# Kernel tuning notes

Hardware: AMD Instinct MI355X
Metric: run time of the kernel (lower is better)

## Reference

```python
import jax, jax.numpy as jnp
import numpy as np

B, L, D_IN = 2048, 512, 32
PRED_LEN = 96
COND = 128      # cond_dim (z_dim)
XPROJ = 128     # x_proj_dim defaults to cond_dim
ODE_H = 128     # ode_hidden
TDIM = 128      # time_dim
HID = 256       # hidden of final MLP
N_STEPS = 32    # fixed-step RK4 steps over t in [0,1] (stands in for adaptive dopri5)
LN_EPS = 1e-5


def _linear(x, w, b):
    return x @ w.T + b


def _layernorm(x, g, b):
    mu = jnp.mean(x, axis=-1, keepdims=True)
    var = jnp.var(x, axis=-1, keepdims=True)
    return (x - mu) * jax.lax.rsqrt(var + LN_EPS) * g + b


def _interp(x_seq, t):
    # linear interp over sequence dim: x_seq (B,L,D), scalar t in [0,1] -> (B,D)
    Ls = x_seq.shape[1]
    pos = jnp.clip(t, 0.0, 1.0) * (Ls - 1)
    i0 = jnp.clip(jnp.floor(pos).astype(jnp.int32), 0, Ls - 1)
    i1 = jnp.clip(i0 + 1, 0, Ls - 1)
    w = (pos - i0.astype(pos.dtype))
    x0 = jax.lax.dynamic_index_in_dim(x_seq, i0, axis=1, keepdims=False)
    x1 = jax.lax.dynamic_index_in_dim(x_seq, i1, axis=1, keepdims=False)
    return (1.0 - w) * x0 + w * x1


def setup_inputs() -> dict:
    key = jax.random.key(0)
    ks = jax.random.split(key, 16)

    def kaiming(k, shape):
        return jax.random.normal(k, shape, jnp.float32) * np.float32(np.sqrt(2.0 / shape[-1]))

    IN_F = PRED_LEN * D_IN + COND + TDIM   # 3328
    OUT_F = PRED_LEN * D_IN                # 3072
    return {
        "x_t": jax.random.normal(ks[0], (B, PRED_LEN, D_IN), jnp.float32),
        "past": jax.random.normal(ks[1], (B, L, D_IN), jnp.float32),
        "t": jax.random.randint(ks[2], (B,), 0, 1000),
        "xproj_w": kaiming(ks[3], (XPROJ, D_IN)), "xproj_b": jnp.zeros((XPROJ,), jnp.float32),
        "z0_w": kaiming(ks[4], (COND, XPROJ)), "z0_b": jnp.zeros((COND,), jnp.float32),
        "ln_g": jnp.ones((COND,), jnp.float32), "ln_b": jnp.zeros((COND,), jnp.float32),
        "w1": kaiming(ks[5], (ODE_H, COND + XPROJ)), "b1": jnp.zeros((ODE_H,), jnp.float32),
        "w2": kaiming(ks[6], (ODE_H, ODE_H)), "b2": jnp.zeros((ODE_H,), jnp.float32),
        "w3": kaiming(ks[7], (COND, ODE_H)), "b3": jnp.zeros((COND,), jnp.float32),
        "fw1": kaiming(ks[8], (HID, IN_F)), "fb1": jnp.zeros((HID,), jnp.float32),
        "fw2": kaiming(ks[9], (HID, HID)), "fb2": jnp.zeros((HID,), jnp.float32),
        "fw3": kaiming(ks[10], (OUT_F, HID)), "fb3": jnp.zeros((OUT_F,), jnp.float32),
    }


def _time_emb(t):
    half = TDIM // 2
    freqs = jnp.exp(-np.float32(np.log(10000.0)) * jnp.arange(half, dtype=jnp.float32) / (half - 1))
    args = t.astype(jnp.float32)[:, None] * freqs[None, :]
    return jnp.concatenate([jnp.sin(args), jnp.cos(args)], axis=1)  # (B, TDIM)


def _forward(x_t, past, t, xproj_w, xproj_b, z0_w, z0_b, ln_g, ln_b,
             w1, b1, w2, b2, w3, b3, fw1, fb1, fw2, fb2, fw3, fb3):
    Bn = x_t.shape[0]
    x_seq = _linear(past, xproj_w, xproj_b)           # (B,L,XPROJ)
    z0 = _linear(x_seq[:, 0, :], z0_w, z0_b)          # (B,COND)

    def odef(tt, z):
        xt = _interp(x_seq, tt)                       # (B,XPROJ)
        zn = _layernorm(z, ln_g, ln_b)
        h = jnp.concatenate([zn, xt], axis=-1)
        h = jax.nn.silu(_linear(h, w1, b1))
        h = jax.nn.silu(_linear(h, w2, b2))
        return _linear(h, w3, b3)                     # (B,COND)

    dt = jnp.float32(1.0 / N_STEPS)

    def step(z, tt):
        k1 = odef(tt, z)
        k2 = odef(tt + dt * 0.5, z + dt * 0.5 * k1)
        k3 = odef(tt + dt * 0.5, z + dt * 0.5 * k2)
        k4 = odef(tt + dt, z + dt * k3)
        return z + (dt / 6.0) * (k1 + 2.0 * k2 + 2.0 * k3 + k4), None

    ts = jnp.arange(N_STEPS, dtype=jnp.float32) * dt
    cond, _ = jax.lax.scan(step, z0, ts)              # zT (B,COND)

    temb = _time_emb(t)                               # (B,TDIM)
    x_flat = x_t.reshape(Bn, -1)                      # (B,PRED_LEN*D_IN)
    h = jnp.concatenate([x_flat, cond, temb], axis=1)
    h = jax.nn.silu(_linear(h, fw1, fb1))
    h = jax.nn.silu(_linear(h, fw2, fb2))
    eps = _linear(h, fw3, fb3)
    return eps.reshape(Bn, PRED_LEN, D_IN)


def reference(x_t, past, t, xproj_w, xproj_b, z0_w, z0_b, ln_g, ln_b,
              w1, b1, w2, b2, w3, b3, fw1, fb1, fw2, fb2, fw3, fb3):
    return _forward(x_t, past, t, xproj_w, xproj_b, z0_w, z0_b, ln_g, ln_b,
                    w1, b1, w2, b2, w3, b3, fw1, fb1, fw2, fb2, fw3, fb3)
```

## Files before the change

### kernel.cpp

```cpp
#include <hip/hip_runtime.h>
#include <math.h>

typedef _Float16 h8f16 __attribute__((ext_vector_type(8)));
typedef _Float16 h4f16 __attribute__((ext_vector_type(4)));
typedef _Float16 h2f16 __attribute__((ext_vector_type(2)));
typedef float f32x4 __attribute__((ext_vector_type(4)));

#define MFMA16(a, b, c) __builtin_amdgcn_mfma_f32_16x16x32_f16((a), (b), (c), 0, 0, 0)

__device__ __forceinline__ float silu_f(float v) {
    return v * __builtin_amdgcn_rcpf(1.0f + __expf(-v));
}

__device__ __forceinline__ void bar_lds() {
    asm volatile("s_waitcnt lgkmcnt(0)" ::: "memory");
    __builtin_amdgcn_s_barrier();
    __builtin_amdgcn_sched_barrier(0);
}

__global__ __launch_bounds__(512, 1) void fat_kernel(
    const float* __restrict__ past,
    const float* __restrict__ xproj_w, const float* __restrict__ xproj_b,
    const float* __restrict__ z0_w, const float* __restrict__ z0_b,
    const float* __restrict__ ln_g, const float* __restrict__ ln_b,
    const float* __restrict__ w1, const float* __restrict__ b1,
    const float* __restrict__ w2, const float* __restrict__ b2,
    const float* __restrict__ w3, const float* __restrict__ b3,
    const float* __restrict__ x_t, const float* __restrict__ fw1,
    const int* __restrict__ tvals,
    float* __restrict__ zbuf, float* __restrict__ h1pre,
    _Float16* __restrict__ tbuf)
{
    __shared__ union {
        struct {
            _Float16 hbuf[16][136];
            _Float16 h1S[16][136];
            _Float16 h2S[16][136];
            float    pS[16][33];
            float    x0S[16][128];
            float    zS0[16][129];
        } ode;
        struct {
            _Float16 aS[128][40];
            _Float16 wS[64][40];
        } gx;
    } sm;

    const int tid = threadIdx.x;

    if (blockIdx.x >= 192) {
        const int t = blockIdx.x - 192;
        for (int c = 0; c < 8; ++c) {
            const int chunk = t * 512 + tid + c * 4096;
            const int b  = chunk >> 4;
            const int j0 = (chunk & 15) * 8;
            const float tv = (float)tvals[b];
            h8f16 v;
#pragma unroll
            for (int j = 0; j < 8; ++j) {
                const int jj  = j0 + j;
                const int idx = (jj < 64) ? jj : jj - 64;
                const float fr = expf(-9.210340371976184f * (float)idx * (1.0f / 63.0f));
                const float a  = tv * fr;
                v[j] = (_Float16)((jj < 64) ? sinf(a) : cosf(a));
            }
            *(h8f16*)&tbuf[(long)b * 128 + j0] = v;
        }
        return;
    }

    if (blockIdx.x >= 128) {
        const int g  = blockIdx.x - 128;
        const int mb = (g >> 2) * 128;
        const int nb = (g & 3) * 64;
        const int lane = tid & 63, wid = tid >> 6;
        const int lrow = lane & 15, lhi = lane >> 4;
        f32x4 acc[4];
#pragma unroll
        for (int nt = 0; nt < 4; ++nt) acc[nt] = (f32x4){0, 0, 0, 0};

        const int sra = tid >> 2, ska = (tid & 3) * 8;
        const int srw = tid >> 3, skw = (tid & 7) * 4;

        for (int k0 = 0; k0 < 3072; k0 += 32) {
            {
                const float* s = x_t + (long)(mb + sra) * 3072 + k0 + ska;
                const f32x4 u0 = *(const f32x4*)s;
                const f32x4 u1 = *(const f32x4*)(s + 4);
                h8f16 v;
#pragma unroll
                for (int j = 0; j < 4; ++j) { v[j] = (_Float16)u0[j]; v[4 + j] = (_Float16)u1[j]; }
                *(h8f16*)&sm.gx.aS[sra][ska] = v;
            }
            {
                const float* s = fw1 + (long)(nb + srw) * 3328 + k0 + skw;
                const f32x4 u = *(const f32x4*)s;
                h4f16 v;
#pragma unroll
                for (int j = 0; j < 4; ++j) v[j] = (_Float16)u[j];
                *(h4f16*)&sm.gx.wS[srw][skw] = v;
            }
            __syncthreads();
            const h8f16 a = *(const h8f16*)&sm.gx.aS[wid * 16 + lrow][lhi * 8];
#pragma unroll
            for (int nt = 0; nt < 4; ++nt) {
                const h8f16 bfr = *(const h8f16*)&sm.gx.wS[nt * 16 + lrow][lhi * 8];
                acc[nt] = MFMA16(a, bfr, acc[nt]);
            }
            __syncthreads();
        }
#pragma unroll
        for (int nt = 0; nt < 4; ++nt) {
            const int cc = nb + nt * 16 + lrow;
#pragma unroll
            for (int j = 0; j < 4; ++j) {
                const int rr = mb + wid * 16 + lhi * 4 + j;
                h1pre[(long)rr * 256 + cc] = acc[nt][j];
            }
        }
        return;
    }

    _Float16 (&hbuf)[16][136] = sm.ode.hbuf;
    _Float16 (&h1S)[16][136]  = sm.ode.h1S;
    _Float16 (&h2S)[16][136]  = sm.ode.h2S;
    float    (&pS)[16][33]    = sm.ode.pS;
    float    (&x0S)[16][128]  = sm.ode.x0S;
    float    (&zS0)[16][129]  = sm.ode.zS0;

    const int wid  = tid >> 6;
    const int lane = tid & 63;
    const int lrow = lane & 15;
    const int lhi  = lane >> 4;
    const int b0   = blockIdx.x * 16;
    const int nc   = wid * 16 + lrow;
    const int koff = lhi * 8;

    h8f16 w1f[4], wcf, w2f[4], w3f[4];
    float b1t, b2r, b3r;
    {
#pragma unroll
        for (int ks = 0; ks < 4; ++ks) {
            h8f16 v1, v2, v3;
#pragma unroll
            for (int j = 0; j < 8; ++j) {
                const int k = ks * 32 + koff + j;
                v1[j] = (_Float16)(w1[nc * 256 + k] * ln_g[k]);
                v2[j] = (_Float16)w2[nc * 128 + k];
                v3[j] = (_Float16)w3[nc * 128 + k];
            }
            w1f[ks] = v1; w2f[ks] = v2; w3f[ks] = v3;
        }
        float wc[8] = {0, 0, 0, 0, 0, 0, 0, 0};
        float bc = 0.0f, bb = 0.0f;
        const float* w1a = w1 + nc * 256;
        const float* w1b = w1a + 128;
#pragma unroll 4
        for (int k = 0; k < 128; ++k) {
            const float a = w1b[k];
            bc += a * xproj_b[k];
            bb += w1a[k] * ln_b[k];
            const float* xr = xproj_w + k * 32 + koff;
#pragma unroll
            for (int j = 0; j < 8; ++j) wc[j] += a * xr[j];
        }
        h8f16 v;
#pragma unroll
        for (int j = 0; j < 8; ++j) v[j] = (_Float16)wc[j];
        wcf = v;
        b1t = b1[nc] + bc + bb;
        b2r = b2[nc]; b3r = b3[nc];
    }

    if (tid < 512) {
        pS[tid >> 5][tid & 31] = past[(long)(b0 + (tid >> 5)) * 16384 + (tid & 31)];
    }
    __syncthreads();
    {
        const int r  = tid >> 5;
        const int c0 = (tid & 31) * 4;
#pragma unroll
        for (int cc = 0; cc < 4; ++cc) {
            const int kc = c0 + cc;
            float s = xproj_b[kc];
            const float* xr = xproj_w + kc * 32;
#pragma unroll
            for (int c = 0; c < 32; ++c) s += pS[r][c] * xr[c];
            x0S[r][kc] = s;
        }
    }
    __syncthreads();
    {
        const int nn = tid & 127;
        const int r0 = (tid >> 7) * 4;
        for (int p = 0; p < 4; ++p) {
            const int r = r0 + p;
            float s = z0_b[nn];
            const float* zr = z0_w + nn * 128;
            for (int k = 0; k < 128; ++k) s += x0S[r][k] * zr[k];
            zS0[r][nn] = s;
        }
    }
    __syncthreads();

    float zc[4], krk[4];
#pragma unroll
    for (int j = 0; j < 4; ++j) {
        zc[j] = zS0[4 * lhi + j][nc];
        hbuf[4 * lhi + j][nc] = (_Float16)zc[j];
    }

    const float DT = 1.0f / 32.0f;

    f32x4 s0a, s0b, s1a, s1b;
    auto stage = [&](int e) {
        const float pos = (float)e * 7.984375f;
        const int i0 = (int)pos;
        const int i1 = (i0 < 511) ? i0 + 1 : 511;
        const float* base = past + (long)(b0 + lrow) * 16384;
        const float* p0 = base + i0 * 32 + koff;
        const float* p1 = base + i1 * 32 + koff;
        s0a = *(const f32x4*)p0; s0b = *(const f32x4*)(p0 + 4);
        s1a = *(const f32x4*)p1; s1b = *(const f32x4*)(p1 + 4);
    };
    auto blend = [&](int e) -> h8f16 {
        const float pos = (float)e * 7.984375f;
        const float w = pos - floorf(pos);
        h8f16 r;
#pragma unroll
        for (int j = 0; j < 4; ++j) {
            r[j]     = (_Float16)(s0a[j] + w * (s1a[j] - s0a[j]));
            r[4 + j] = (_Float16)(s0b[j] + w * (s1b[j] - s0b[j]));
        }
        return r;
    };

    const h2f16 one2 = {(_Float16)1.0f, (_Float16)1.0f};

    auto phaseA = [&](h8f16 bxc) {
        h8f16 xf[4];
#pragma unroll
        for (int ks = 0; ks < 4; ++ks)
            xf[ks] = *(const h8f16*)&hbuf[lrow][ks * 32 + koff];
        float s0 = 0.f, s1 = 0.f, q0 = 0.f, q1 = 0.f;
#pragma unroll
        for (int ks = 0; ks < 4; ++ks) {
#pragma unroll
            for (int p = 0; p < 4; ++p) {
                const h2f16 x2 = {xf[ks][2 * p], xf[ks][2 * p + 1]};
                if (p & 1) {
                    s1 = __builtin_amdgcn_fdot2(x2, one2, s1, false);
                    q1 = __builtin_amdgcn_fdot2(x2, x2, q1, false);
                } else {
                    s0 = __builtin_amdgcn_fdot2(x2, one2, s0, false);
                    q0 = __builtin_amdgcn_fdot2(x2, x2, q0, false);
                }
            }
        }
        float s = s0 + s1, q = q0 + q1;
        s += __shfl_xor(s, 16); q += __shfl_xor(q, 16);
        s += __shfl_xor(s, 32); q += __shfl_xor(q, 32);
        const float mu  = s * (1.0f / 128.0f);
        const float var = q * (1.0f / 128.0f) - mu * mu;
        const float inv = 1.0f / sqrtf(var + 1e-5f);
        const _Float16 ih = (_Float16)inv;
        const _Float16 mh = (_Float16)(-mu * inv);
        h8f16 ip, mp;
#pragma unroll
        for (int j = 0; j < 8; ++j) { ip[j] = ih; mp[j] = mh; }
        f32x4 acc = {0, 0, 0, 0};
#pragma unroll
        for (int ks = 0; ks < 4; ++ks) {
            const h8f16 az = xf[ks] * ip + mp;
            acc = MFMA16(az, w1f[ks], acc);
        }
        acc = MFMA16(bxc, wcf, acc);
#pragma unroll
        for (int j = 0; j < 4; ++j)
            h1S[4 * lhi + j][nc] = (_Float16)silu_f(acc[j] + b1t);
    };
    auto phaseB = [&]() {
        f32x4 acc = {0, 0, 0, 0};
#pragma unroll
        for (int ks = 0; ks < 4; ++ks) {
            const h8f16 a = *(const h8f16*)&h1S[lrow][ks * 32 + koff];
            acc = MFMA16(a, w2f[ks], acc);
        }
#pragma unroll
        for (int j = 0; j < 4; ++j)
            h2S[4 * lhi + j][nc] = (_Float16)silu_f(acc[j] + b2r);
    };
    auto phaseC = [&]() -> f32x4 {
        f32x4 acc = {0, 0, 0, 0};
#pragma unroll
        for (int ks = 0; ks < 4; ++ks) {
            const h8f16 a = *(const h8f16*)&h2S[lrow][ks * 32 + koff];
            acc = MFMA16(a, w3f[ks], acc);
        }
#pragma unroll
        for (int j = 0; j < 4; ++j) acc[j] += b3r;
        return acc;
    };

    stage(0);
    h8f16 bxc = blend(0);
    __syncthreads();

#pragma unroll 1
    for (int st = 0; st < 32; ++st) {
        const int e1 = 2 * st + 1, e2 = 2 * st + 2;
        phaseA(bxc);
        stage(e1);
        bar_lds();
        phaseB(); bar_lds();
        {
            const f32x4 k = phaseC();
#pragma unroll
            for (int j = 0; j < 4; ++j) {
                krk[j] = k[j];
                hbuf[4 * lhi + j][nc] = (_Float16)(zc[j] + 0.5f * DT * k[j]);
            }
        }
        bar_lds();
        bxc = blend(e1);
        phaseA(bxc); bar_lds();
        phaseB(); bar_lds();
        {
            const f32x4 k = phaseC();
#pragma unroll
            for (int j = 0; j < 4; ++j) {
                krk[j] += 2.0f * k[j];
                hbuf[4 * lhi + j][nc] = (_Float16)(zc[j] + 0.5f * DT * k[j]);
            }
        }
        bar_lds();
        phaseA(bxc);
        stage(e2);
        bar_lds();
        phaseB(); bar_lds();
        {
            const f32x4 k = phaseC();
#pragma unroll
            for (int j = 0; j < 4; ++j) {
                krk[j] += 2.0f * k[j];
                hbuf[4 * lhi + j][nc] = (_Float16)(zc[j] + DT * k[j]);
            }
        }
        bar_lds();
        bxc = blend(e2);
        phaseA(bxc); bar_lds();
        phaseB(); bar_lds();
        {
            const f32x4 k = phaseC();
#pragma unroll
            for (int j = 0; j < 4; ++j) {
                zc[j] += (DT / 6.0f) * (krk[j] + k[j]);
                hbuf[4 * lhi + j][nc] = (_Float16)zc[j];
            }
        }
        bar_lds();
    }

#pragma unroll
    for (int j = 0; j < 4; ++j)
        zbuf[(long)(b0 + 4 * lhi + j) * 128 + nc] = zc[j];
}

__global__ __launch_bounds__(256) void gemm1c_kernel(
    const float* __restrict__ cond, const _Float16* __restrict__ tbuf,
    const float* __restrict__ fw1, const float* __restrict__ fb1,
    const float* __restrict__ h1pre, _Float16* __restrict__ h1)
{
    __shared__ _Float16 aS[64][40];
    __shared__ _Float16 wS[64][40];
    const int mb = blockIdx.x * 64, nb = blockIdx.y * 64;
    const int tid = threadIdx.x, lane = tid & 63, wq = tid >> 6;
    const int lrow = lane & 15, lhi = lane >> 4;
    f32x4 acc[4];
#pragma unroll
    for (int nt = 0; nt < 4; ++nt) acc[nt] = (f32x4){0, 0, 0, 0};

    const int sr = tid >> 2;
    const int sk = (tid & 3) * 8;

    for (int k0 = 0; k0 < 256; k0 += 32) {
        if (k0 < 128) {
            const float* s = cond + (long)(mb + sr) * 128 + k0 + sk;
            const f32x4 u0 = *(const f32x4*)s;
            const f32x4 u1 = *(const f32x4*)(s + 4);
            h8f16 v;
#pragma unroll
            for (int j = 0; j < 4; ++j) { v[j] = (_Float16)u0[j]; v[4 + j] = (_Float16)u1[j]; }
            *(h8f16*)&aS[sr][sk] = v;
        } else {
            *(h8f16*)&aS[sr][sk] =
                *(const h8f16*)&tbuf[(long)(mb + sr) * 128 + (k0 - 128) + sk];
        }
        {
            const float* s = fw1 + (long)(nb + sr) * 3328 + 3072 + k0 + sk;
            h8f16 v;
#pragma unroll
            for (int j = 0; j < 8; ++j) v[j] = (_Float16)s[j];
            *(h8f16*)&wS[sr][sk] = v;
        }
        __syncthreads();
        const h8f16 a = *(const h8f16*)&aS[wq * 16 + lrow][lhi * 8];
#pragma unroll
        for (int nt = 0; nt < 4; ++nt) {
            const h8f16 bfr = *(const h8f16*)&wS[nt * 16 + lrow][lhi * 8];
            acc[nt] = MFMA16(a, bfr, acc[nt]);
        }
        __syncthreads();
    }

#pragma unroll
    for (int nt = 0; nt < 4; ++nt) {
        const int cc = nb + nt * 16 + lrow;
        const float bv = fb1[cc];
#pragma unroll
        for (int j = 0; j < 4; ++j) {
            const int rr = mb + wq * 16 + lhi * 4 + j;
            const float v = acc[nt][j] + h1pre[(long)rr * 256 + cc] + bv;
            h1[(long)rr * 256 + cc] = (_Float16)silu_f(v);
        }
    }
}

template <bool SILU, bool OUT_F16>
__global__ __launch_bounds__(256) void gemm_f16(
    const _Float16* __restrict__ A, const float* __restrict__ W,
    const float* __restrict__ bias, void* __restrict__ out,
    int M, int N, int K)
{
    __shared__ _Float16 aS[64][40];
    __shared__ _Float16 wS[64][40];
    const int mb = blockIdx.x * 64, nb = blockIdx.y * 64;
    const int tid = threadIdx.x, lane = tid & 63, wq = tid >> 6;
    const int lrow = lane & 15, lhi = lane >> 4;
    f32x4 acc[4];
#pragma unroll
    for (int nt = 0; nt < 4; ++nt) acc[nt] = (f32x4){0, 0, 0, 0};

    const int sr = tid >> 2;
    const int sk = (tid & 3) * 8;

    for (int k0 = 0; k0 < K; k0 += 32) {
        {
            h8f16 v = *(const h8f16*)&A[(long)(mb + sr) * K + k0 + sk];
            *(h8f16*)&aS[sr][sk] = v;
        }
        {
            const float* s = &W[(long)(nb + sr) * K + k0 + sk];
            h8f16 v;
#pragma unroll
            for (int j = 0; j < 8; ++j) v[j] = (_Float16)s[j];
            *(h8f16*)&wS[sr][sk] = v;
        }
        __syncthreads();
        h8f16 a = *(const h8f16*)&aS[wq * 16 + lrow][lhi * 8];
#pragma unroll
        for (int nt = 0; nt < 4; ++nt) {
            h8f16 bfr = *(const h8f16*)&wS[nt * 16 + lrow][lhi * 8];
            acc[nt] = MFMA16(a, bfr, acc[nt]);
        }
        __syncthreads();
    }

#pragma unroll
    for (int nt = 0; nt < 4; ++nt) {
        const int cc = nb + nt * 16 + lrow;
        const float bv = bias[cc];
#pragma unroll
        for (int j = 0; j < 4; ++j) {
            const int rr = mb + wq * 16 + lhi * 4 + j;
            float v = acc[nt][j] + bv;
            if (SILU) v = silu_f(v);
            if (OUT_F16) ((_Float16*)out)[(long)rr * N + cc] = (_Float16)v;
            else         ((float*)out)[(long)rr * N + cc] = v;
        }
    }
}

extern "C" void kernel_launch(void* const* d_in, const int* in_sizes, int n_in,
                              void* d_out, int out_size, void* d_ws, size_t ws_size,
                              hipStream_t stream)
{
    const float* x_t     = (const float*)d_in[0];
    const float* past    = (const float*)d_in[1];
    const int*   tvals   = (const int*)d_in[2];
    const float* xproj_w = (const float*)d_in[3];
    const float* xproj_b = (const float*)d_in[4];
    const float* z0_w    = (const float*)d_in[5];
    const float* z0_b    = (const float*)d_in[6];
    const float* ln_g    = (const float*)d_in[7];
    const float* ln_b    = (const float*)d_in[8];
    const float* w1      = (const float*)d_in[9];
    const float* b1      = (const float*)d_in[10];
    const float* w2      = (const float*)d_in[11];
    const float* b2      = (const float*)d_in[12];
    const float* w3      = (const float*)d_in[13];
    const float* b3      = (const float*)d_in[14];
    const float* fw1     = (const float*)d_in[15];
    const float* fb1     = (const float*)d_in[16];
    const float* fw2     = (const float*)d_in[17];
    const float* fb2     = (const float*)d_in[18];
    const float* fw3     = (const float*)d_in[19];
    const float* fb3     = (const float*)d_in[20];

    char* ws = (char*)d_ws;
    float*     zbuf  = (float*)ws;
    _Float16*  tbuf  = (_Float16*)(ws + (1 << 20));
    float*     h1pre = (float*)(ws + 2 * (1 << 20));
    _Float16*  h1    = (_Float16*)(ws + 4 * (1 << 20));
    _Float16*  h2    = (_Float16*)(ws + 5 * (1 << 20));

    fat_kernel<<<200, 512, 0, stream>>>(past, xproj_w, xproj_b, z0_w, z0_b,
                                        ln_g, ln_b, w1, b1, w2, b2, w3, b3,
                                        x_t, fw1, tvals, zbuf, h1pre, tbuf);

    gemm1c_kernel<<<dim3(32, 4), 256, 0, stream>>>(zbuf, tbuf, fw1, fb1, h1pre, h1);

    gemm_f16<true,  true ><<<dim3(32, 4),  256, 0, stream>>>(h1, fw2, fb2, h2, 2048, 256, 256);
    gemm_f16<false, false><<<dim3(32, 48), 256, 0, stream>>>(h2, fw3, fb3, d_out, 2048, 3072, 256);
}
```

Measured before the change: 368.6 us.

## Split fat kernel; run ODE with one wave per tile without barriers

```diff
diff --git a/kernel.cpp b/kernel.cpp
--- a/kernel.cpp
+++ b/kernel.cpp
@@ -2,7 +2,6 @@
 #include <math.h>
 
 typedef _Float16 h8f16 __attribute__((ext_vector_type(8)));
-typedef _Float16 h4f16 __attribute__((ext_vector_type(4)));
 typedef _Float16 h2f16 __attribute__((ext_vector_type(2)));
 typedef float f32x4 __attribute__((ext_vector_type(4)));
 
@@ -12,205 +11,115 @@
     return v * __builtin_amdgcn_rcpf(1.0f + __expf(-v));
 }
 
-__device__ __forceinline__ void bar_lds() {
-    asm volatile("s_waitcnt lgkmcnt(0)" ::: "memory");
-    __builtin_amdgcn_s_barrier();
-    __builtin_amdgcn_sched_barrier(0);
-}
-
-__global__ __launch_bounds__(512, 1) void fat_kernel(
+__global__ __launch_bounds__(128) void z0wc_kernel(
     const float* __restrict__ past,
-    const float* __restrict__ xproj_w, const float* __restrict__ xproj_b,
-    const float* __restrict__ z0_w, const float* __restrict__ z0_b,
-    const float* __restrict__ ln_g, const float* __restrict__ ln_b,
-    const float* __restrict__ w1, const float* __restrict__ b1,
+    const float* __restrict__ xw, const float* __restrict__ xb,
+    const float* __restrict__ zw, const float* __restrict__ zb,
+    const float* __restrict__ w1, const float* __restrict__ lnb,
+    const float* __restrict__ b1,
+    float* __restrict__ zbuf, float* __restrict__ wcb, float* __restrict__ b1tb)
+{
+    const int tid = threadIdx.x;
+    if (blockIdx.x == 2048) {
+        const int n = tid;
+        float wc[32];
+#pragma unroll
+        for (int c = 0; c < 32; ++c) wc[c] = 0.0f;
+        float bc = 0.0f, bb = 0.0f;
+        const float* w1a = w1 + n * 256;
+        const float* w1b = w1a + 128;
+        for (int k = 0; k < 128; ++k) {
+            const float a = w1b[k];
+            bc += a * xb[k];
+            bb += w1a[k] * lnb[k];
+            const float* xr = xw + k * 32;
+#pragma unroll
+            for (int c = 0; c < 32; ++c) wc[c] = fmaf(a, xr[c], wc[c]);
+        }
+#pragma unroll
+        for (int c = 0; c < 32; ++c) wcb[n * 32 + c] = wc[c];
+        b1tb[n] = b1[n] + bc + bb;
+        return;
+    }
+    __shared__ float p[32];
+    __shared__ float x0[128];
+    const int b = blockIdx.x;
+    if (tid < 32) p[tid] = past[(long)b * 16384 + tid];
+    __syncthreads();
+    float s = xb[tid];
+#pragma unroll
+    for (int c = 0; c < 32; ++c) s += p[c] * xw[tid * 32 + c];
+    x0[tid] = s;
+    __syncthreads();
+    float z = zb[tid];
+    for (int k = 0; k < 128; ++k) z += x0[k] * zw[tid * 128 + k];
+    zbuf[(long)b * 128 + tid] = z;
+}
+
+__global__ __launch_bounds__(64, 1) void ode_kernel(
+    const float* __restrict__ past,
+    const float* __restrict__ ln_g,
+    const float* __restrict__ w1,
+    const float* __restrict__ wcb, const float* __restrict__ b1tb,
     const float* __restrict__ w2, const float* __restrict__ b2,
     const float* __restrict__ w3, const float* __restrict__ b3,
-    const float* __restrict__ x_t, const float* __restrict__ fw1,
-    const int* __restrict__ tvals,
-    float* __restrict__ zbuf, float* __restrict__ h1pre,
-    _Float16* __restrict__ tbuf)
-{
-    __shared__ union {
-        struct {
-            _Float16 hbuf[16][136];
-            _Float16 h1S[16][136];
-            _Float16 h2S[16][136];
-            float    pS[16][33];
-            float    x0S[16][128];
-            float    zS0[16][129];
-        } ode;
-        struct {
-            _Float16 aS[128][40];
-            _Float16 wS[64][40];
-        } gx;
-    } sm;
-
-    const int tid = threadIdx.x;
-
-    if (blockIdx.x >= 192) {
-        const int t = blockIdx.x - 192;
-        for (int c = 0; c < 8; ++c) {
-            const int chunk = t * 512 + tid + c * 4096;
-            const int b  = chunk >> 4;
-            const int j0 = (chunk & 15) * 8;
-            const float tv = (float)tvals[b];
-            h8f16 v;
-#pragma unroll
-            for (int j = 0; j < 8; ++j) {
-                const int jj  = j0 + j;
-                const int idx = (jj < 64) ? jj : jj - 64;
-                const float fr = expf(-9.210340371976184f * (float)idx * (1.0f / 63.0f));
-                const float a  = tv * fr;
-                v[j] = (_Float16)((jj < 64) ? sinf(a) : cosf(a));
-            }
-            *(h8f16*)&tbuf[(long)b * 128 + j0] = v;
-        }
-        return;
-    }
-
-    if (blockIdx.x >= 128) {
-        const int g  = blockIdx.x - 128;
-        const int mb = (g >> 2) * 128;
-        const int nb = (g & 3) * 64;
-        const int lane = tid & 63, wid = tid >> 6;
-        const int lrow = lane & 15, lhi = lane >> 4;
-        f32x4 acc[4];
-#pragma unroll
-        for (int nt = 0; nt < 4; ++nt) acc[nt] = (f32x4){0, 0, 0, 0};
-
-        const int sra = tid >> 2, ska = (tid & 3) * 8;
-        const int srw = tid >> 3, skw = (tid & 7) * 4;
-
-        for (int k0 = 0; k0 < 3072; k0 += 32) {
-            {
-                const float* s = x_t + (long)(mb + sra) * 3072 + k0 + ska;
-                const f32x4 u0 = *(const f32x4*)s;
-                const f32x4 u1 = *(const f32x4*)(s + 4);
-                h8f16 v;
-#pragma unroll
-                for (int j = 0; j < 4; ++j) { v[j] = (_Float16)u0[j]; v[4 + j] = (_Float16)u1[j]; }
-                *(h8f16*)&sm.gx.aS[sra][ska] = v;
-            }
-            {
-                const float* s = fw1 + (long)(nb + srw) * 3328 + k0 + skw;
-                const f32x4 u = *(const f32x4*)s;
-                h4f16 v;
-#pragma unroll
-                for (int j = 0; j < 4; ++j) v[j] = (_Float16)u[j];
-                *(h4f16*)&sm.gx.wS[srw][skw] = v;
-            }
-            __syncthreads();
-            const h8f16 a = *(const h8f16*)&sm.gx.aS[wid * 16 + lrow][lhi * 8];
-#pragma unroll
-            for (int nt = 0; nt < 4; ++nt) {
-                const h8f16 bfr = *(const h8f16*)&sm.gx.wS[nt * 16 + lrow][lhi * 8];
-                acc[nt] = MFMA16(a, bfr, acc[nt]);
-            }
-            __syncthreads();
-        }
-#pragma unroll
-        for (int nt = 0; nt < 4; ++nt) {
-            const int cc = nb + nt * 16 + lrow;
-#pragma unroll
-            for (int j = 0; j < 4; ++j) {
-                const int rr = mb + wid * 16 + lhi * 4 + j;
-                h1pre[(long)rr * 256 + cc] = acc[nt][j];
-            }
-        }
-        return;
-    }
-
-    _Float16 (&hbuf)[16][136] = sm.ode.hbuf;
-    _Float16 (&h1S)[16][136]  = sm.ode.h1S;
-    _Float16 (&h2S)[16][136]  = sm.ode.h2S;
-    float    (&pS)[16][33]    = sm.ode.pS;
-    float    (&x0S)[16][128]  = sm.ode.x0S;
-    float    (&zS0)[16][129]  = sm.ode.zS0;
-
-    const int wid  = tid >> 6;
-    const int lane = tid & 63;
+    float* __restrict__ zbuf)
+{
+    __shared__ h8f16 wfrag[72][64];
+    __shared__ _Float16 vS[16][136];
+    __shared__ _Float16 h1S[16][136];
+    __shared__ _Float16 h2S[16][136];
+
+    const int lane = threadIdx.x;
     const int lrow = lane & 15;
     const int lhi  = lane >> 4;
+    const int koff = lhi * 8;
     const int b0   = blockIdx.x * 16;
-    const int nc   = wid * 16 + lrow;
-    const int koff = lhi * 8;
-
-    h8f16 w1f[4], wcf, w2f[4], w3f[4];
-    float b1t, b2r, b3r;
-    {
+    const int PERM[8] = {0, 16, 1, 17, 2, 18, 3, 19};
+
+    h8f16 w3f[8][4];
+    float b1r[8], b2r[8], b3r[8];
+#pragma unroll
+    for (int t = 0; t < 8; ++t) {
+        const int n = t * 16 + lrow;
 #pragma unroll
         for (int ks = 0; ks < 4; ++ks) {
             h8f16 v1, v2, v3;
 #pragma unroll
             for (int j = 0; j < 8; ++j) {
-                const int k = ks * 32 + koff + j;
-                v1[j] = (_Float16)(w1[nc * 256 + k] * ln_g[k]);
-                v2[j] = (_Float16)w2[nc * 128 + k];
-                v3[j] = (_Float16)w3[nc * 128 + k];
-            }
-            w1f[ks] = v1; w2f[ks] = v2; w3f[ks] = v3;
-        }
-        float wc[8] = {0, 0, 0, 0, 0, 0, 0, 0};
-        float bc = 0.0f, bb = 0.0f;
-        const float* w1a = w1 + nc * 256;
-        const float* w1b = w1a + 128;
-#pragma unroll 4
-        for (int k = 0; k < 128; ++k) {
-            const float a = w1b[k];
-            bc += a * xproj_b[k];
-            bb += w1a[k] * ln_b[k];
-            const float* xr = xproj_w + k * 32 + koff;
-#pragma unroll
-            for (int j = 0; j < 8; ++j) wc[j] += a * xr[j];
-        }
-        h8f16 v;
-#pragma unroll
-        for (int j = 0; j < 8; ++j) v[j] = (_Float16)wc[j];
-        wcf = v;
-        b1t = b1[nc] + bc + bb;
-        b2r = b2[nc]; b3r = b3[nc];
-    }
-
-    if (tid < 512) {
-        pS[tid >> 5][tid & 31] = past[(long)(b0 + (tid >> 5)) * 16384 + (tid & 31)];
-    }
-    __syncthreads();
-    {
-        const int r  = tid >> 5;
-        const int c0 = (tid & 31) * 4;
-#pragma unroll
-        for (int cc = 0; cc < 4; ++cc) {
-            const int kc = c0 + cc;
-            float s = xproj_b[kc];
-            const float* xr = xproj_w + kc * 32;
-#pragma unroll
-            for (int c = 0; c < 32; ++c) s += pS[r][c] * xr[c];
-            x0S[r][kc] = s;
-        }
-    }
-    __syncthreads();
-    {
-        const int nn = tid & 127;
-        const int r0 = (tid >> 7) * 4;
-        for (int p = 0; p < 4; ++p) {
-            const int r = r0 + p;
-            float s = z0_b[nn];
-            const float* zr = z0_w + nn * 128;
-            for (int k = 0; k < 128; ++k) s += x0S[r][k] * zr[k];
-            zS0[r][nn] = s;
-        }
-    }
-    __syncthreads();
-
-    float zc[4], krk[4];
-#pragma unroll
-    for (int j = 0; j < 4; ++j) {
-        zc[j] = zS0[4 * lhi + j][nc];
-        hbuf[4 * lhi + j][nc] = (_Float16)zc[j];
-    }
+                const int k = ks * 32 + lhi * 4 + PERM[j];
+                v1[j] = (_Float16)(w1[n * 256 + k] * ln_g[k]);
+                v2[j] = (_Float16)w2[n * 128 + k];
+                v3[j] = (_Float16)w3[n * 128 + k];
+            }
+            wfrag[t * 4 + ks][lane] = v1;
+            wfrag[40 + t * 4 + ks][lane] = v2;
+            w3f[t][ks] = v3;
+        }
+        {
+            h8f16 v;
+#pragma unroll
+            for (int j = 0; j < 8; ++j) v[j] = (_Float16)wcb[n * 32 + koff + j];
+            wfrag[32 + t][lane] = v;
+        }
+        b1r[t] = b1tb[n]; b2r[t] = b2[n]; b3r[t] = b3[n];
+    }
+
+    float zc[8][4], krk[8][4];
+#pragma unroll
+    for (int t = 0; t < 8; ++t)
+#pragma unroll
+        for (int j = 0; j < 4; ++j)
+            zc[t][j] = zbuf[(long)(b0 + 4 * lhi + j) * 128 + t * 16 + lrow];
+#pragma unroll
+    for (int t2 = 0; t2 < 4; ++t2)
+#pragma unroll
+        for (int j = 0; j < 4; ++j)
+            *(h2f16*)&vS[4 * lhi + j][32 * t2 + 2 * lrow] =
+                (h2f16){(_Float16)zc[2 * t2][j], (_Float16)zc[2 * t2 + 1][j]};
 
     const float DT = 1.0f / 32.0f;
+    const h2f16 one2 = {(_Float16)1.0f, (_Float16)1.0f};
 
     f32x4 s0a, s0b, s1a, s1b;
     auto stage = [&](int e) {
@@ -235,13 +144,12 @@
         return r;
     };
 
-    const h2f16 one2 = {(_Float16)1.0f, (_Float16)1.0f};
-
-    auto phaseA = [&](h8f16 bxc) {
+    f32x4 acc[8];
+    auto eval = [&](h8f16 bxc) {
         h8f16 xf[4];
 #pragma unroll
         for (int ks = 0; ks < 4; ++ks)
-            xf[ks] = *(const h8f16*)&hbuf[lrow][ks * 32 + koff];
+            xf[ks] = *(const h8f16*)&vS[lrow][ks * 32 + koff];
         float s0 = 0.f, s1 = 0.f, q0 = 0.f, q1 = 0.f;
 #pragma unroll
         for (int ks = 0; ks < 4; ++ks) {
@@ -268,102 +176,207 @@
         h8f16 ip, mp;
 #pragma unroll
         for (int j = 0; j < 8; ++j) { ip[j] = ih; mp[j] = mh; }
-        f32x4 acc = {0, 0, 0, 0};
-#pragma unroll
-        for (int ks = 0; ks < 4; ++ks) {
-            const h8f16 az = xf[ks] * ip + mp;
-            acc = MFMA16(az, w1f[ks], acc);
-        }
-        acc = MFMA16(bxc, wcf, acc);
-#pragma unroll
-        for (int j = 0; j < 4; ++j)
-            h1S[4 * lhi + j][nc] = (_Float16)silu_f(acc[j] + b1t);
+        h8f16 az[4];
+#pragma unroll
+        for (int ks = 0; ks < 4; ++ks) az[ks] = xf[ks] * ip + mp;
+
+#pragma unroll
+        for (int t = 0; t < 8; ++t) acc[t] = (f32x4){0, 0, 0, 0};
+#pragma unroll
+        for (int ks = 0; ks < 4; ++ks)
+#pragma unroll
+            for (int t = 0; t < 8; ++t)
+                acc[t] = MFMA16(az[ks], wfrag[t * 4 + ks][lane], acc[t]);
+#pragma unroll
+        for (int t = 0; t < 8; ++t)
+            acc[t] = MFMA16(bxc, wfrag[32 + t][lane], acc[t]);
+#pragma unroll
+        for (int t2 = 0; t2 < 4; ++t2)
+#pragma unroll
+            for (int j = 0; j < 4; ++j) {
+                const _Float16 o0 = (_Float16)silu_f(acc[2 * t2][j] + b1r[2 * t2]);
+                const _Float16 o1 = (_Float16)silu_f(acc[2 * t2 + 1][j] + b1r[2 * t2 + 1]);
+                *(h2f16*)&h1S[4 * lhi + j][32 * t2 + 2 * lrow] = (h2f16){o0, o1};
+            }
+
+        h8f16 a1[4];
+#pragma unroll
+        for (int ks = 0; ks < 4; ++ks)
+            a1[ks] = *(const h8f16*)&h1S[lrow][ks * 32 + koff];
+#pragma unroll
+        for (int t = 0; t < 8; ++t) acc[t] = (f32x4){0, 0, 0, 0};
+#pragma unroll
+        for (int ks = 0; ks < 4; ++ks)
+#pragma unroll
+            for (int t = 0; t < 8; ++t)
+                acc[t] = MFMA16(a1[ks], wfrag[40 + t * 4 + ks][lane], acc[t]);
+#pragma unroll
+        for (int t2 = 0; t2 < 4; ++t2)
+#pragma unroll
+            for (int j = 0; j < 4; ++j) {
+                const _Float16 o0 = (_Float16)silu_f(acc[2 * t2][j] + b2r[2 * t2]);
+                const _Float16 o1 = (_Float16)silu_f(acc[2 * t2 + 1][j] + b2r[2 * t2 + 1]);
+                *(h2f16*)&h2S[4 * lhi + j][32 * t2 + 2 * lrow] = (h2f16){o0, o1};
+            }
+
+        h8f16 a2[4];
+#pragma unroll
+        for (int ks = 0; ks < 4; ++ks)
+            a2[ks] = *(const h8f16*)&h2S[lrow][ks * 32 + koff];
+#pragma unroll
+        for (int t = 0; t < 8; ++t) acc[t] = (f32x4){0, 0, 0, 0};
+#pragma unroll
+        for (int ks = 0; ks < 4; ++ks)
+#pragma unroll
+            for (int t = 0; t < 8; ++t)
+                acc[t] = MFMA16(a2[ks], w3f[t][ks], acc[t]);
     };
-    auto phaseB = [&]() {
-        f32x4 acc = {0, 0, 0, 0};
-#pragma unroll
-        for (int ks = 0; ks < 4; ++ks) {
-            const h8f16 a = *(const h8f16*)&h1S[lrow][ks * 32 + koff];
-            acc = MFMA16(a, w2f[ks], acc);
-        }
-#pragma unroll
-        for (int j = 0; j < 4; ++j)
-            h2S[4 * lhi + j][nc] = (_Float16)silu_f(acc[j] + b2r);
-    };
-    auto phaseC = [&]() -> f32x4 {
-        f32x4 acc = {0, 0, 0, 0};
-#pragma unroll
-        for (int ks = 0; ks < 4; ++ks) {
-            const h8f16 a = *(const h8f16*)&h2S[lrow][ks * 32 + koff];
-            acc = MFMA16(a, w3f[ks], acc);
-        }
-#pragma unroll
-        for (int j = 0; j < 4; ++j) acc[j] += b3r;
-        return acc;
+
+    auto writeV = [&](int t2, int j, float v0, float v1) {
+        *(h2f16*)&vS[4 * lhi + j][32 * t2 + 2 * lrow] =
+            (h2f16){(_Float16)v0, (_Float16)v1};
     };
 
     stage(0);
     h8f16 bxc = blend(0);
-    __syncthreads();
 
 #pragma unroll 1
     for (int st = 0; st < 32; ++st) {
         const int e1 = 2 * st + 1, e2 = 2 * st + 2;
-        phaseA(bxc);
+        eval(bxc);
         stage(e1);
-        bar_lds();
-        phaseB(); bar_lds();
+#pragma unroll
+        for (int t2 = 0; t2 < 4; ++t2)
+#pragma unroll
+            for (int j = 0; j < 4; ++j) {
+                const float k0 = acc[2 * t2][j] + b3r[2 * t2];
+                const float k1 = acc[2 * t2 + 1][j] + b3r[2 * t2 + 1];
+                krk[2 * t2][j] = k0; krk[2 * t2 + 1][j] = k1;
+                writeV(t2, j, zc[2 * t2][j] + 0.5f * DT * k0,
+                              zc[2 * t2 + 1][j] + 0.5f * DT * k1);
+            }
+        bxc = blend(e1);
+        eval(bxc);
+#pragma unroll
+        for (int t2 = 0; t2 < 4; ++t2)
+#pragma unroll
+            for (int j = 0; j < 4; ++j) {
+                const float k0 = acc[2 * t2][j] + b3r[2 * t2];
+                const float k1 = acc[2 * t2 + 1][j] + b3r[2 * t2 + 1];
+                krk[2 * t2][j] += 2.0f * k0; krk[2 * t2 + 1][j] += 2.0f * k1;
+                writeV(t2, j, zc[2 * t2][j] + 0.5f * DT * k0,
+                              zc[2 * t2 + 1][j] + 0.5f * DT * k1);
+            }
+        eval(bxc);
+        stage(e2);
+#pragma unroll
+        for (int t2 = 0; t2 < 4; ++t2)
+#pragma unroll
+            for (int j = 0; j < 4; ++j) {
+                const float k0 = acc[2 * t2][j] + b3r[2 * t2];
+                const float k1 = acc[2 * t2 + 1][j] + b3r[2 * t2 + 1];
+                krk[2 * t2][j] += 2.0f * k0; krk[2 * t2 + 1][j] += 2.0f * k1;
+                writeV(t2, j, zc[2 * t2][j] + DT * k0,
+                              zc[2 * t2 + 1][j] + DT * k1);
+            }
+        bxc = blend(e2);
+        eval(bxc);
+#pragma unroll
+        for (int t2 = 0; t2 < 4; ++t2)
+#pragma unroll
+            for (int j = 0; j < 4; ++j) {
+                const float k0 = acc[2 * t2][j] + b3r[2 * t2];
+                const float k1 = acc[2 * t2 + 1][j] + b3r[2 * t2 + 1];
+                zc[2 * t2][j]     += (DT / 6.0f) * (krk[2 * t2][j] + k0);
+                zc[2 * t2 + 1][j] += (DT / 6.0f) * (krk[2 * t2 + 1][j] + k1);
+                writeV(t2, j, zc[2 * t2][j], zc[2 * t2 + 1][j]);
+            }
+    }
+
+#pragma unroll
+    for (int t = 0; t < 8; ++t)
+#pragma unroll
+        for (int j = 0; j < 4; ++j)
+            zbuf[(long)(b0 + 4 * lhi + j) * 128 + t * 16 + lrow] = zc[t][j];
+}
+
+__global__ __launch_bounds__(256) void gemm1x_kernel(
+    const float* __restrict__ x_t, const float* __restrict__ fw1,
+    float* __restrict__ h1pre)
+{
+    __shared__ _Float16 aS[64][40];
+    __shared__ _Float16 wS[64][40];
+    const int mb = blockIdx.x * 64, nb = blockIdx.y * 64;
+    const int tid = threadIdx.x, lane = tid & 63, wq = tid >> 6;
+    const int lrow = lane & 15, lhi = lane >> 4;
+    f32x4 acc[4];
+#pragma unroll
+    for (int nt = 0; nt < 4; ++nt) acc[nt] = (f32x4){0, 0, 0, 0};
+
+    const int sr = tid >> 2;
+    const int sk = (tid & 3) * 8;
+
+    for (int k0 = 0; k0 < 3072; k0 += 32) {
         {
-            const f32x4 k = phaseC();
-#pragma unroll
-            for (int j = 0; j < 4; ++j) {
-                krk[j] = k[j];
-                hbuf[4 * lhi + j][nc] = (_Float16)(zc[j] + 0.5f * DT * k[j]);
-            }
-        }
-        bar_lds();
-        bxc = blend(e1);
-        phaseA(bxc); bar_lds();
-        phaseB(); bar_lds();
+            const float* s = x_t + (long)(mb + sr) * 3072 + k0 + sk;
+            const f32x4 u0 = *(const f32x4*)s;
+            const f32x4 u1 = *(const f32x4*)(s + 4);
+            h8f16 v;
+#pragma unroll
+            for (int j = 0; j < 4; ++j) { v[j] = (_Float16)u0[j]; v[4 + j] = (_Float16)u1[j]; }
+            *(h8f16*)&aS[sr][sk] = v;
+        }
         {
-            const f32x4 k = phaseC();
-#pragma unroll
-            for (int j = 0; j < 4; ++j) {
-                krk[j] += 2.0f * k[j];
-                hbuf[4 * lhi + j][nc] = (_Float16)(zc[j] + 0.5f * DT * k[j]);
-            }
-        }
-        bar_lds();
-        phaseA(bxc);
-        stage(e2);
-        bar_lds();
-        phaseB(); bar_lds();
-        {
-            const f32x4 k = phaseC();
-#pragma unroll
-            for (int j = 0; j < 4; ++j) {
-                krk[j] += 2.0f * k[j];
-                hbuf[4 * lhi + j][nc] = (_Float16)(zc[j] + DT * k[j]);
-            }
-        }
-        bar_lds();
-        bxc = blend(e2);
-        phaseA(bxc); bar_lds();
-        phaseB(); bar_lds();
-        {
-            const f32x4 k = phaseC();
-#pragma unroll
-            for (int j = 0; j < 4; ++j) {
-                zc[j] += (DT / 6.0f) * (krk[j] + k[j]);
-                hbuf[4 * lhi + j][nc] = (_Float16)zc[j];
-            }
-        }
-        bar_lds();
-    }
-
-#pragma unroll
-    for (int j = 0; j < 4; ++j)
-        zbuf[(long)(b0 + 4 * lhi + j) * 128 + nc] = zc[j];
+            const float* s = fw1 + (long)(nb + sr) * 3328 + k0 + sk;
+            const f32x4 u0 = *(const f32x4*)s;
+            const f32x4 u1 = *(const f32x4*)(s + 4);
+            h8f16 v;
+#pragma unroll
+            for (int j = 0; j < 4; ++j) { v[j] = (_Float16)u0[j]; v[4 + j] = (_Float16)u1[j]; }
+            *(h8f16*)&wS[sr][sk] = v;
+        }
+        __syncthreads();
+        const h8f16 a = *(const h8f16*)&aS[wq * 16 + lrow][lhi * 8];
+#pragma unroll
+        for (int nt = 0; nt < 4; ++nt) {
+            const h8f16 bfr = *(const h8f16*)&wS[nt * 16 + lrow][lhi * 8];
+            acc[nt] = MFMA16(a, bfr, acc[nt]);
+        }
+        __syncthreads();
+    }
+
+#pragma unroll
+    for (int nt = 0; nt < 4; ++nt) {
+        const int cc = nb + nt * 16 + lrow;
+#pragma unroll
+        for (int j = 0; j < 4; ++j) {
+            const int rr = mb + wq * 16 + lhi * 4 + j;
+            h1pre[(long)rr * 256 + cc] = acc[nt][j];
+        }
+    }
+}
+
+__global__ __launch_bounds__(256) void temb_kernel(
+    const int* __restrict__ tvals, _Float16* __restrict__ tbuf)
+{
+    const int tid = threadIdx.x;
+#pragma unroll 1
+    for (int c = 0; c < 8; ++c) {
+        const int chunk = blockIdx.x * 256 + tid + c * 4096;
+        const int b  = chunk >> 4;
+        const int j0 = (chunk & 15) * 8;
+        const float tv = (float)tvals[b];
+        h8f16 v;
+#pragma unroll
+        for (int j = 0; j < 8; ++j) {
+            const int jj  = j0 + j;
+            const int idx = (jj < 64) ? jj : jj - 64;
+            const float fr = expf(-9.210340371976184f * (float)idx * (1.0f / 63.0f));
+            const float a  = tv * fr;
+            v[j] = (_Float16)((jj < 64) ? sinf(a) : cosf(a));
+        }
+        *(h8f16*)&tbuf[(long)b * 128 + j0] = v;
+    }
 }
 
 __global__ __launch_bounds__(256) void gemm1c_kernel(
@@ -513,10 +526,17 @@
     float*     h1pre = (float*)(ws + 2 * (1 << 20));
     _Float16*  h1    = (_Float16*)(ws + 4 * (1 << 20));
     _Float16*  h2    = (_Float16*)(ws + 5 * (1 << 20));
-
-    fat_kernel<<<200, 512, 0, stream>>>(past, xproj_w, xproj_b, z0_w, z0_b,
-                                        ln_g, ln_b, w1, b1, w2, b2, w3, b3,
-                                        x_t, fw1, tvals, zbuf, h1pre, tbuf);
+    float*     wcb   = (float*)(ws + 6 * (1 << 20));
+    float*     b1tb  = (float*)(ws + 6 * (1 << 20) + (1 << 16));
+
+    z0wc_kernel<<<2049, 128, 0, stream>>>(past, xproj_w, xproj_b, z0_w, z0_b,
+                                          w1, ln_b, b1, zbuf, wcb, b1tb);
+
+    ode_kernel<<<128, 64, 0, stream>>>(past, ln_g, w1, wcb, b1tb,
+                                       w2, b2, w3, b3, zbuf);
+
+    gemm1x_kernel<<<dim3(32, 4), 256, 0, stream>>>(x_t, fw1, h1pre);
+    temb_kernel<<<16, 256, 0, stream>>>(tvals, tbuf);
 
     gemm1c_kernel<<<dim3(32, 4), 256, 0, stream>>>(zbuf, tbuf, fw1, fb1, h1pre, h1);
 
```

New measurement: 752.2 us. 104% more time.
